# Kernel tuning notes

Hardware: AMD Instinct MI355X
Metric: run time of the kernel (lower is better)

## Reference

```python
import jax, jax.numpy as jnp
import numpy as np

# --- static config (matches init_kwargs / input_specs) ---
N_GRAPHS = 32
NODES = 1000          # num_nodes per graph
N = N_GRAPHS * NODES  # 32000 total nodes
F_IN = 128            # num_features
E_DIM = 16            # edge_attr_dim
H, C = 4, 16          # heads, GAT_dim
HC = H * C            # 64
E = 512000            # edges (before self-loops)
PROJ = 8              # proj_nodes
OUT = 256             # output_dim
NEG_SLOPE = 0.2       # PyG GATConv default


def setup_inputs() -> dict:
    key = jax.random.key(0)
    ks = jax.random.split(key, 20)
    s = 0.1
    return {
        "x": jax.random.normal(ks[0], (N, F_IN), jnp.float32),
        "edge_attr": jax.random.normal(ks[1], (E, E_DIM), jnp.float32),
        # layer 0 (input_conv): F_IN -> H*C
        "W0":   jax.random.normal(ks[2], (F_IN, HC), jnp.float32) * s,
        "a_s0": jax.random.normal(ks[3], (H, C), jnp.float32) * s,
        "a_d0": jax.random.normal(ks[4], (H, C), jnp.float32) * s,
        "W_e0": jax.random.normal(ks[5], (E_DIM, HC), jnp.float32) * s,
        "a_e0": jax.random.normal(ks[6], (H, C), jnp.float32) * s,
        "b0":   jnp.zeros((HC,), jnp.float32),
        # layers 1..2 stacked: HC -> H*C
        "Wg":   jax.random.normal(ks[7], (2, HC, HC), jnp.float32) * s,
        "a_sg": jax.random.normal(ks[8], (2, H, C), jnp.float32) * s,
        "a_dg": jax.random.normal(ks[9], (2, H, C), jnp.float32) * s,
        "W_eg": jax.random.normal(ks[10], (2, E_DIM, HC), jnp.float32) * s,
        "a_eg": jax.random.normal(ks[11], (2, H, C), jnp.float32) * s,
        "bg":   jnp.zeros((2, HC), jnp.float32),
        # node_proj: HC -> PROJ ; fc_out: NODES*PROJ -> OUT
        "Wp": jax.random.normal(ks[12], (HC, PROJ), jnp.float32) * s,
        "bp": jnp.zeros((PROJ,), jnp.float32),
        "Wo": jax.random.normal(ks[13], (NODES * PROJ, OUT), jnp.float32) * (s / 4),
        "bo": jnp.zeros((OUT,), jnp.float32),
        "edge_index": jax.random.randint(ks[14], (2, E), 0, N, jnp.int32),
        "batch": jnp.repeat(jnp.arange(N_GRAPHS, dtype=jnp.int32), NODES),
    }


def _gat_layer(x, src, dst, eattr, W, a_s, a_d, W_e, a_e, b):
    """PyG GATConv (concat=True, shared src/dst lin, edge_dim) forward."""
    xl = (x @ W).reshape(N, H, C)                       # [N,H,C]
    al_s = jnp.sum(xl * a_s, axis=-1)                   # [N,H]
    al_d = jnp.sum(xl * a_d, axis=-1)                   # [N,H]
    el = (eattr @ W_e).reshape(-1, H, C)                # [Ef,H,C]
    al_e = jnp.sum(el * a_e, axis=-1)                   # [Ef,H]
    logits = jax.nn.leaky_relu(al_s[src] + al_d[dst] + al_e, NEG_SLOPE)
    # segment softmax over destination nodes (every node has a self-loop)
    mx = jax.ops.segment_max(logits, dst, num_segments=N)
    p = jnp.exp(logits - mx[dst])
    denom = jax.ops.segment_sum(p, dst, num_segments=N)
    alpha = p / denom[dst]                               # [Ef,H]
    out = jax.ops.segment_sum(xl[src] * alpha[..., None], dst, num_segments=N)
    return out.reshape(N, HC) + b


def reference(x, edge_attr, W0, a_s0, a_d0, W_e0, a_e0, b0,
              Wg, a_sg, a_dg, W_eg, a_eg, bg,
              Wp, bp, Wo, bo, edge_index, batch):
    src, dst = edge_index[0], edge_index[1]
    # PyG add_self_loops with fill_value='mean': per-dst mean of incoming edge_attr
    deg = jax.ops.segment_sum(jnp.ones((E,), edge_attr.dtype), dst, num_segments=N)
    loop_attr = jax.ops.segment_sum(edge_attr, dst, num_segments=N) / jnp.maximum(deg, 1.0)[:, None]
    loops = jnp.arange(N, dtype=src.dtype)
    src_f = jnp.concatenate([src, loops])
    dst_f = jnp.concatenate([dst, loops])
    ea_f = jnp.concatenate([edge_attr, loop_attr], axis=0)   # [E+N, E_DIM]

    h = jax.nn.relu(_gat_layer(x, src_f, dst_f, ea_f, W0, a_s0, a_d0, W_e0, a_e0, b0))
    for i in range(2):
        h = jax.nn.relu(_gat_layer(h, src_f, dst_f, ea_f,
                                   Wg[i], a_sg[i], a_dg[i], W_eg[i], a_eg[i], bg[i]))
    h = jax.nn.relu(h @ Wp + bp)                             # [N, PROJ]
    B = batch.shape[0] // NODES                              # static batch count
    h = h.reshape(B, NODES * PROJ)
    return h @ Wo + bo                                       # [B, OUT]
```

## Files before the change

### kernel.cpp

```cpp
#include <hip/hip_runtime.h>
#include <hip/hip_bf16.h>
#include <hip/hip_fp16.h>

#define N_NODES 32000
#define FIN     128
#define E_EDGES 512000
#define EF_EDGES 544000
#define HC      64
#define NGRAPH  32
#define PROJ    8
#define OUT_DIM 256

static __device__ inline unsigned short f2bf(float f) {
  unsigned int x = __float_as_uint(f);
  unsigned int r = (x + 0x7fffu + ((x >> 16) & 1u)) >> 16;
  return (unsigned short)r;
}
static __device__ inline float bf2f(unsigned short u) {
  return __uint_as_float((unsigned int)u << 16);
}
static __device__ inline unsigned short f2h(float f) {
  return __half_as_ushort(__float2half(f));
}
static __device__ inline float h2f(unsigned short u) {
  return __half2float(__ushort_as_half(u));
}

__global__ __launch_bounds__(256) void zero_kernel(int* __restrict__ deg) {
  deg[blockIdx.x * 256 + threadIdx.x] = 0;
}

__global__ __launch_bounds__(256) void deg_kernel(const int* __restrict__ ei,
                                                  int* __restrict__ deg) {
  int e = blockIdx.x * 256 + threadIdx.x;
  atomicAdd(&deg[ei[E_EDGES + e]], 1);
}

__global__ __launch_bounds__(256) void scan1_kernel(const int* __restrict__ deg,
                                                    int* __restrict__ offs,
                                                    int* __restrict__ bsum) {
  int idx = blockIdx.x * 256 + threadIdx.x;
  int lane = threadIdx.x & 63;
  int w = threadIdx.x >> 6;
  int v = deg[idx] + 1;
  int s = v;
#pragma unroll
  for (int off = 1; off < 64; off <<= 1) {
    int t = __shfl_up(s, off);
    if (lane >= off) s += t;
  }
  __shared__ int wsum[4];
  if (lane == 63) wsum[w] = s;
  __syncthreads();
  int add = 0;
#pragma unroll
  for (int i = 0; i < 4; ++i) add += (i < w) ? wsum[i] : 0;
  int incl = s + add;
  offs[idx] = incl - v;
  if (threadIdx.x == 255) bsum[blockIdx.x] = incl;
}

__global__ __launch_bounds__(256) void scan3_kernel(const int* __restrict__ bsum,
                                                    int* __restrict__ offs,
                                                    int* __restrict__ nxt) {
  __shared__ int wsum[4];
  int tid = threadIdx.x, bid = blockIdx.x;
  int lane = tid & 63, w = tid >> 6;
  int v = (tid < bid) ? bsum[tid] : 0;
#pragma unroll
  for (int off = 1; off < 64; off <<= 1) v += __shfl_xor(v, off);
  if (lane == 0) wsum[w] = v;
  __syncthreads();
  int boff = wsum[0] + wsum[1] + wsum[2] + wsum[3];
  int idx = bid * 256 + tid;
  int o = offs[idx] + boff;
  offs[idx] = o;
  nxt[idx] = o;
  if (bid == 0 && tid == 0) offs[N_NODES] = EF_EDGES;
}

__global__ __launch_bounds__(256) void fill_kernel(const int* __restrict__ ei,
                                                   int* __restrict__ nxt,
                                                   int* __restrict__ csr_src,
                                                   int* __restrict__ csr_eid) {
  int e = blockIdx.x * 256 + threadIdx.x;
  int s, d;
  if (e < E_EDGES) { s = ei[e]; d = ei[E_EDGES + e]; }
  else             { s = e - E_EDGES; d = s; }
  int pos = atomicAdd(&nxt[d], 1);
  csr_src[pos] = s;
  csr_eid[pos] = e;
}

__device__ __forceinline__ void compute_Me(float (*sMe)[16][4],
                                           const float* __restrict__ W_e0,
                                           const float* __restrict__ a_e0,
                                           const float* __restrict__ W_eg,
                                           const float* __restrict__ a_eg) {
  int tid = threadIdx.x;
  if (tid < 192) {
    int l = tid >> 6, r6 = tid & 63, d = r6 >> 2, h = r6 & 3;
    const float* We = (l == 0) ? W_e0 : W_eg + (size_t)(l - 1) * 16 * HC;
    const float* ae = (l == 0) ? a_e0 : a_eg + (size_t)(l - 1) * 64;
    float s = 0.f;
#pragma unroll
    for (int c = 0; c < 16; ++c) s += We[d * HC + h * 16 + c] * ae[h * 16 + c];
    sMe[l][d][h] = s;
  }
  __syncthreads();
}

__global__ __launch_bounds__(256) void edge_kernel(const float* __restrict__ edge_attr,
                                                   const float* __restrict__ W_e0,
                                                   const float* __restrict__ a_e0,
                                                   const float* __restrict__ W_eg,
                                                   const float* __restrict__ a_eg,
                                                   const int* __restrict__ offs,
                                                   const int* __restrict__ csr_eid,
                                                   unsigned short* __restrict__ lgE) {
  __shared__ float sMe[3][16][4];
  __shared__ float sMean[4][16];
  compute_Me(sMe, W_e0, a_e0, W_eg, a_eg);
  int b = blockIdx.x;
  int tid = threadIdx.x;
  if (b < 8000) {
    int lane = tid & 63, wv = tid >> 6;
    int n = b * 4 + wv;
    int k = lane & 15, g = lane >> 4;
    int beg = offs[n], end = offs[n + 1];
    float s = 0.f;
    int posl = -1;
    for (int i = beg + g; i < end; i += 4) {
      int e = csr_eid[i];
      if (e < E_EDGES) s += edge_attr[(size_t)e * 16 + k];
      else posl = i;
    }
    s += __shfl_xor(s, 16);
    s += __shfl_xor(s, 32);
    posl = max(posl, __shfl_xor(posl, 16));
    posl = max(posl, __shfl_xor(posl, 32));
    int degv = end - beg - 1;
    float mean = s / fmaxf((float)degv, 1.f);
    if (g == 0) sMean[wv][k] = mean;
    if (lane < 3) {
      int l = lane;
      float r0 = 0.f, r1 = 0.f, r2 = 0.f, r3 = 0.f;
#pragma unroll
      for (int d = 0; d < 16; ++d) {
        float a = sMean[wv][d];
        r0 = fmaf(a, sMe[l][d][0], r0);
        r1 = fmaf(a, sMe[l][d][1], r1);
        r2 = fmaf(a, sMe[l][d][2], r2);
        r3 = fmaf(a, sMe[l][d][3], r3);
      }
      unsigned long long u =
          (unsigned long long)f2h(r0) |
          ((unsigned long long)f2h(r1) << 16) |
          ((unsigned long long)f2h(r2) << 32) |
          ((unsigned long long)f2h(r3) << 48);
      *(unsigned long long*)&lgE[((size_t)l * EF_EDGES + posl) * 4] = u;
    }
  } else {
    int pos = (b - 8000) * 256 + tid;
    int e = csr_eid[pos];
    if (e < E_EDGES) {
      float av[16];
      *(float4*)&av[0]  = *(const float4*)&edge_attr[(size_t)e * 16 + 0];
      *(float4*)&av[4]  = *(const float4*)&edge_attr[(size_t)e * 16 + 4];
      *(float4*)&av[8]  = *(const float4*)&edge_attr[(size_t)e * 16 + 8];
      *(float4*)&av[12] = *(const float4*)&edge_attr[(size_t)e * 16 + 12];
#pragma unroll
      for (int l = 0; l < 3; ++l) {
        float r0 = 0.f, r1 = 0.f, r2 = 0.f, r3 = 0.f;
#pragma unroll
        for (int d = 0; d < 16; ++d) {
          float a = av[d];
          r0 = fmaf(a, sMe[l][d][0], r0);
          r1 = fmaf(a, sMe[l][d][1], r1);
          r2 = fmaf(a, sMe[l][d][2], r2);
          r3 = fmaf(a, sMe[l][d][3], r3);
        }
        unsigned long long u =
            (unsigned long long)f2h(r0) |
            ((unsigned long long)f2h(r1) << 16) |
            ((unsigned long long)f2h(r2) << 32) |
            ((unsigned long long)f2h(r3) << 48);
        __builtin_nontemporal_store(
            u, (unsigned long long*)&lgE[((size_t)l * EF_EDGES + pos) * 4]);
      }
    }
  }
}

template <int K>
__global__ __launch_bounds__(256) void transform_kernel(const float* __restrict__ A,
                                                        const float* __restrict__ W,
                                                        const float* __restrict__ a_s,
                                                        const float* __restrict__ a_d,
                                                        unsigned short* __restrict__ xlb,
                                                        float* __restrict__ al_s,
                                                        float* __restrict__ al_d) {
  __shared__ float sW[64][64];
  __shared__ float sA[64][65];
  int tid = threadIdx.x;
  int row0 = blockIdx.x * 64;
  int tx = tid & 15, ty = tid >> 4;
  int c0 = tx * 4, r0 = ty * 4;
  float acc[4][4] = {};
  for (int kc = 0; kc < K; kc += 64) {
    for (int i = tid; i < 1024; i += 256) {
      int kk = i >> 4, c4 = (i & 15) * 4;
      *(float4*)&sW[kk][c4] = *(const float4*)&W[(size_t)(kc + kk) * HC + c4];
    }
    for (int i = tid; i < 1024; i += 256) {
      int r = i >> 4, k4 = (i & 15) * 4;
      float4 v = *(const float4*)&A[(size_t)(row0 + r) * K + kc + k4];
      sA[r][k4 + 0] = v.x; sA[r][k4 + 1] = v.y;
      sA[r][k4 + 2] = v.z; sA[r][k4 + 3] = v.w;
    }
    __syncthreads();
#pragma unroll 8
    for (int kk = 0; kk < 64; ++kk) {
      float4 w = *(float4*)&sW[kk][c0];
      float a0 = sA[r0 + 0][kk];
      float a1 = sA[r0 + 1][kk];
      float a2 = sA[r0 + 2][kk];
      float a3 = sA[r0 + 3][kk];
      acc[0][0] = fmaf(a0, w.x, acc[0][0]); acc[0][1] = fmaf(a0, w.y, acc[0][1]);
      acc[0][2] = fmaf(a0, w.z, acc[0][2]); acc[0][3] = fmaf(a0, w.w, acc[0][3]);
      acc[1][0] = fmaf(a1, w.x, acc[1][0]); acc[1][1] = fmaf(a1, w.y, acc[1][1]);
      acc[1][2] = fmaf(a1, w.z, acc[1][2]); acc[1][3] = fmaf(a1, w.w, acc[1][3]);
      acc[2][0] = fmaf(a2, w.x, acc[2][0]); acc[2][1] = fmaf(a2, w.y, acc[2][1]);
      acc[2][2] = fmaf(a2, w.z, acc[2][2]); acc[2][3] = fmaf(a2, w.w, acc[2][3]);
      acc[3][0] = fmaf(a3, w.x, acc[3][0]); acc[3][1] = fmaf(a3, w.y, acc[3][1]);
      acc[3][2] = fmaf(a3, w.z, acc[3][2]); acc[3][3] = fmaf(a3, w.w, acc[3][3]);
    }
    __syncthreads();
  }
  float asv[4], adv[4];
#pragma unroll
  for (int j = 0; j < 4; ++j) { asv[j] = a_s[c0 + j]; adv[j] = a_d[c0 + j]; }
  int hd = tx >> 2;
#pragma unroll
  for (int i = 0; i < 4; ++i) {
    int r = row0 + r0 + i;
    ushort4 u = make_ushort4(f2bf(acc[i][0]), f2bf(acc[i][1]),
                             f2bf(acc[i][2]), f2bf(acc[i][3]));
    *(ushort4*)&xlb[(size_t)r * HC + c0] = u;
    float ps = acc[i][0] * asv[0] + acc[i][1] * asv[1] + acc[i][2] * asv[2] + acc[i][3] * asv[3];
    float pd = acc[i][0] * adv[0] + acc[i][1] * adv[1] + acc[i][2] * adv[2] + acc[i][3] * adv[3];
    ps += __shfl_xor(ps, 1); ps += __shfl_xor(ps, 2);
    pd += __shfl_xor(pd, 1); pd += __shfl_xor(pd, 2);
    if ((tx & 3) == 0) {
      al_s[(size_t)r * 4 + hd] = ps;
      al_d[(size_t)r * 4 + hd] = pd;
    }
  }
}

template <int FUSE_PROJ>
__global__ __launch_bounds__(256) void gather_kernel(const int* __restrict__ offs,
                                                     const int* __restrict__ csr_src,
                                                     const unsigned short* __restrict__ lg,
                                                     const unsigned short* __restrict__ xlb,
                                                     const float* __restrict__ al_s,
                                                     const float* __restrict__ al_d,
                                                     const float* __restrict__ bias,
                                                     const float* __restrict__ Wp,
                                                     const float* __restrict__ bp,
                                                     float* __restrict__ outp) {
  int tid = threadIdx.x;
  int lane = tid & 63;
  int n = blockIdx.x * 4 + (tid >> 6);
  int u = lane & 31;
  int hf = lane >> 5;
  int c0 = u * 2;
  int hd = u >> 3;
  int beg = offs[n], end = offs[n + 1];
  float ald = al_d[(size_t)n * 4 + hd];
  float m = -1e30f, denom = 0.f, a0 = 0.f, a1 = 0.f;
  int ib = beg;
  for (; ib + 8 <= end; ib += 8) {
    int j0 = ib + hf, j1 = j0 + 2, j2 = j0 + 4, j3 = j0 + 6;
    int s0 = csr_src[j0];
    int s1 = csr_src[j1];
    int s2 = csr_src[j2];
    int s3 = csr_src[j3];
    unsigned short g0 = lg[(size_t)j0 * 4 + hd];
    unsigned short g1 = lg[(size_t)j1 * 4 + hd];
    unsigned short g2 = lg[(size_t)j2 * 4 + hd];
    unsigned short g3 = lg[(size_t)j3 * 4 + hd];
    unsigned int x0 = *(const unsigned int*)&xlb[(size_t)s0 * HC + c0];
    unsigned int x1 = *(const unsigned int*)&xlb[(size_t)s1 * HC + c0];
    unsigned int x2 = *(const unsigned int*)&xlb[(size_t)s2 * HC + c0];
    unsigned int x3 = *(const unsigned int*)&xlb[(size_t)s3 * HC + c0];
    float l0 = h2f(g0) + al_s[(size_t)s0 * 4 + hd] + ald;
    float l1 = h2f(g1) + al_s[(size_t)s1 * 4 + hd] + ald;
    float l2 = h2f(g2) + al_s[(size_t)s2 * 4 + hd] + ald;
    float l3 = h2f(g3) + al_s[(size_t)s3 * 4 + hd] + ald;
    l0 = (l0 > 0.f) ? l0 : 0.2f * l0;
    l1 = (l1 > 0.f) ? l1 : 0.2f * l1;
    l2 = (l2 > 0.f) ? l2 : 0.2f * l2;
    l3 = (l3 > 0.f) ? l3 : 0.2f * l3;
    float mx = fmaxf(fmaxf(fmaxf(l0, l1), fmaxf(l2, l3)), m);
    float sc = __expf(m - mx);
    float p0 = __expf(l0 - mx);
    float p1 = __expf(l1 - mx);
    float p2 = __expf(l2 - mx);
    float p3 = __expf(l3 - mx);
    denom = denom * sc + ((p0 + p1) + (p2 + p3));
    a0 = a0 * sc + p0 * bf2f((unsigned short)(x0 & 0xffff))
                 + p1 * bf2f((unsigned short)(x1 & 0xffff))
                 + p2 * bf2f((unsigned short)(x2 & 0xffff))
                 + p3 * bf2f((unsigned short)(x3 & 0xffff));
    a1 = a1 * sc + p0 * bf2f((unsigned short)(x0 >> 16))
                 + p1 * bf2f((unsigned short)(x1 >> 16))
                 + p2 * bf2f((unsigned short)(x2 >> 16))
                 + p3 * bf2f((unsigned short)(x3 >> 16));
    m = mx;
  }
  for (int j = ib + hf; j < end; j += 2) {
    int s = csr_src[j];
    unsigned short g = lg[(size_t)j * 4 + hd];
    unsigned int xx = *(const unsigned int*)&xlb[(size_t)s * HC + c0];
    float l = h2f(g) + al_s[(size_t)s * 4 + hd] + ald;
    l = (l > 0.f) ? l : 0.2f * l;
    float mx = fmaxf(m, l);
    float sc = __expf(m - mx);
    float pp = __expf(l - mx);
    denom = denom * sc + pp;
    a0 = a0 * sc + pp * bf2f((unsigned short)(xx & 0xffff));
    a1 = a1 * sc + pp * bf2f((unsigned short)(xx >> 16));
    m = mx;
  }
  float m2 = __shfl_xor(m, 32);
  float d2 = __shfl_xor(denom, 32);
  float b0 = __shfl_xor(a0, 32);
  float b1 = __shfl_xor(a1, 32);
  float mm = fmaxf(m, m2);
  float sA = __expf(m - mm), sB = __expf(m2 - mm);
  denom = denom * sA + d2 * sB;
  a0 = a0 * sA + b0 * sB;
  a1 = a1 * sA + b1 * sB;
  float hv0 = fmaxf(a0 / denom + bias[c0], 0.f);
  float hv1 = fmaxf(a1 / denom + bias[c0 + 1], 0.f);
  if constexpr (!FUSE_PROJ) {
    if (hf == 0) {
      float2 o; o.x = hv0; o.y = hv1;
      *(float2*)&outp[(size_t)n * HC + c0] = o;
    }
  } else {
    float pj[8];
#pragma unroll
    for (int j = 0; j < 8; ++j)
      pj[j] = (hf == 0) ? hv0 * Wp[c0 * PROJ + j] + hv1 * Wp[(c0 + 1) * PROJ + j] : 0.f;
#pragma unroll
    for (int off = 1; off < 64; off <<= 1) {
#pragma unroll
      for (int j = 0; j < 8; ++j) pj[j] += __shfl_xor(pj[j], off);
    }
    if (lane < 8) {
      float v = pj[0];
      v = (lane == 1) ? pj[1] : v;
      v = (lane == 2) ? pj[2] : v;
      v = (lane == 3) ? pj[3] : v;
      v = (lane == 4) ? pj[4] : v;
      v = (lane == 5) ? pj[5] : v;
      v = (lane == 6) ? pj[6] : v;
      v = (lane == 7) ? pj[7] : v;
      outp[(size_t)n * PROJ + lane] = fmaxf(v + bp[lane], 0.f);
    }
  }
}

__global__ __launch_bounds__(256) void fc1_kernel(const float* __restrict__ p,
                                                  const float* __restrict__ Wo,
                                                  float* __restrict__ part) {
  __shared__ float sp[NGRAPH][250];
  int kc = blockIdx.x;
  int ct = blockIdx.y;
  int tid = threadIdx.x;
  for (int i = tid; i < NGRAPH * 250; i += 256) {
    int g = i / 250, kk = i % 250;
    sp[g][kk] = p[(size_t)g * 8000 + kc * 250 + kk];
  }
  __syncthreads();
  int c = ct * 64 + (tid & 63);
  int kg = tid >> 6;
  float acc[NGRAPH] = {};
  for (int kk = kg; kk < 250; kk += 4) {
    float w = __builtin_nontemporal_load(&Wo[(size_t)(kc * 250 + kk) * OUT_DIM + c]);
#pragma unroll
    for (int g = 0; g < NGRAPH; ++g) acc[g] = fmaf(sp[g][kk], w, acc[g]);
  }
  int ch = kc * 4 + kg;
#pragma unroll
  for (int g = 0; g < NGRAPH; ++g)
    part[((size_t)ch * NGRAPH + g) * OUT_DIM + c] = acc[g];
}

__global__ __launch_bounds__(256) void fc2_kernel(const float* __restrict__ part,
                                                  const float* __restrict__ bo,
                                                  float* __restrict__ out) {
  int i = blockIdx.x * 256 + threadIdx.x;
  int g = i >> 8, c = i & 255;
  float s = bo[c];
  for (int ch = 0; ch < 128; ++ch) s += part[((size_t)ch * NGRAPH + g) * OUT_DIM + c];
  out[i] = s;
}

extern "C" void kernel_launch(void* const* d_in, const int* in_sizes, int n_in,
                              void* d_out, int out_size, void* d_ws, size_t ws_size,
                              hipStream_t stream) {
  const float* x         = (const float*)d_in[0];
  const float* edge_attr = (const float*)d_in[1];
  const float* W0        = (const float*)d_in[2];
  const float* a_s0      = (const float*)d_in[3];
  const float* a_d0      = (const float*)d_in[4];
  const float* W_e0      = (const float*)d_in[5];
  const float* a_e0      = (const float*)d_in[6];
  const float* b0        = (const float*)d_in[7];
  const float* Wg        = (const float*)d_in[8];
  const float* a_sg      = (const float*)d_in[9];
  const float* a_dg      = (const float*)d_in[10];
  const float* W_eg      = (const float*)d_in[11];
  const float* a_eg      = (const float*)d_in[12];
  const float* bg        = (const float*)d_in[13];
  const float* Wp        = (const float*)d_in[14];
  const float* bp        = (const float*)d_in[15];
  const float* Wo        = (const float*)d_in[16];
  const float* bo        = (const float*)d_in[17];
  const int*   ei        = (const int*)d_in[18];

  char* base = (char*)d_ws;
  size_t off = 0;
  auto alloc = [&](size_t bytes) -> void* {
    void* ptr = base + off;
    off = (off + bytes + 255) & ~(size_t)255;
    return ptr;
  };
  int*            deg     = (int*)alloc((size_t)N_NODES * 4);
  int*            offs    = (int*)alloc((size_t)(N_NODES + 1) * 4);
  int*            nxt     = (int*)alloc((size_t)N_NODES * 4);
  int*            bsum    = (int*)alloc(128 * 4);
  int*            csr_src = (int*)alloc((size_t)EF_EDGES * 4);
  int*            csr_eid = (int*)alloc((size_t)EF_EDGES * 4);
  unsigned short* lgE     = (unsigned short*)alloc((size_t)3 * EF_EDGES * 4 * 2);
  unsigned short* xlb     = (unsigned short*)alloc((size_t)N_NODES * HC * 2);
  float*          al_s    = (float*)alloc((size_t)N_NODES * 4 * 4);
  float*          al_d    = (float*)alloc((size_t)N_NODES * 4 * 4);
  float*          hA      = (float*)alloc((size_t)N_NODES * HC * 4);
  float*          hB      = (float*)alloc((size_t)N_NODES * HC * 4);
  float*          pbuf    = (float*)alloc((size_t)N_NODES * PROJ * 4);
  float*          part    = (float*)alloc((size_t)128 * NGRAPH * OUT_DIM * 4);

  zero_kernel<<<N_NODES / 256, 256, 0, stream>>>(deg);
  deg_kernel<<<E_EDGES / 256, 256, 0, stream>>>(ei, deg);
  scan1_kernel<<<N_NODES / 256, 256, 0, stream>>>(deg, offs, bsum);
  scan3_kernel<<<N_NODES / 256, 256, 0, stream>>>(bsum, offs, nxt);
  fill_kernel<<<EF_EDGES / 256, 256, 0, stream>>>(ei, nxt, csr_src, csr_eid);
  edge_kernel<<<8000 + 2125, 256, 0, stream>>>(edge_attr, W_e0, a_e0, W_eg, a_eg,
                                               offs, csr_eid, lgE);
  transform_kernel<FIN><<<N_NODES / 64, 256, 0, stream>>>(x, W0, a_s0, a_d0, xlb, al_s, al_d);

  gather_kernel<0><<<N_NODES / 4, 256, 0, stream>>>(offs, csr_src, lgE, xlb,
                                                    al_s, al_d, b0, Wp, bp, hA);
  transform_kernel<HC><<<N_NODES / 64, 256, 0, stream>>>(hA, Wg, a_sg, a_dg, xlb, al_s, al_d);
  gather_kernel<0><<<N_NODES / 4, 256, 0, stream>>>(offs, csr_src, lgE + (size_t)EF_EDGES * 4,
                                                    xlb, al_s, al_d, bg, Wp, bp, hB);
  transform_kernel<HC><<<N_NODES / 64, 256, 0, stream>>>(hB, Wg + HC * HC, a_sg + 64,
                                                         a_dg + 64, xlb, al_s, al_d);
  gather_kernel<1><<<N_NODES / 4, 256, 0, stream>>>(offs, csr_src, lgE + (size_t)2 * EF_EDGES * 4,
                                                    xlb, al_s, al_d, bg + 64, Wp, bp, pbuf);

  fc1_kernel<<<dim3(32, 4), 256, 0, stream>>>(pbuf, Wo, part);
  fc2_kernel<<<NGRAPH, 256, 0, stream>>>(part, bo, (float*)d_out);
}
```

Before: 274.5 us.

## Pack source attention scores into feature rows and drop online softmax max

Stores the per-head source attention logit inside each node's bf16 feature row, padded to a stride of 72, so the gather reads features and al_s from the same row instead of from two separate arrays. The softmax no longer subtracts a running maximum, which removes the rescaling exps and lets the half-wave merge become a plain sum. The edge loop is unrolled to 16 edges per iteration, with loads batched ahead of the math to raise memory-level parallelism. The risk is overflow in exp if logits grow large, since there is no max subtraction.

New measurement: 278.6 us. No clear change (+1.5%).

```diff
diff --git a/kernel.cpp b/kernel.cpp
--- a/kernel.cpp
+++ b/kernel.cpp
@@ -7,6 +7,7 @@
 #define E_EDGES 512000
 #define EF_EDGES 544000
 #define HC      64
+#define XSTR    72
 #define NGRAPH  32
 #define PROJ    8
 #define OUT_DIM 256
@@ -198,7 +199,6 @@
                                                         const float* __restrict__ a_s,
                                                         const float* __restrict__ a_d,
                                                         unsigned short* __restrict__ xlb,
-                                                        float* __restrict__ al_s,
                                                         float* __restrict__ al_d) {
   __shared__ float sW[64][64];
   __shared__ float sA[64][65];
@@ -246,13 +246,13 @@
     int r = row0 + r0 + i;
     ushort4 u = make_ushort4(f2bf(acc[i][0]), f2bf(acc[i][1]),
                              f2bf(acc[i][2]), f2bf(acc[i][3]));
-    *(ushort4*)&xlb[(size_t)r * HC + c0] = u;
+    *(ushort4*)&xlb[(size_t)r * XSTR + c0] = u;
     float ps = acc[i][0] * asv[0] + acc[i][1] * asv[1] + acc[i][2] * asv[2] + acc[i][3] * asv[3];
     float pd = acc[i][0] * adv[0] + acc[i][1] * adv[1] + acc[i][2] * adv[2] + acc[i][3] * adv[3];
     ps += __shfl_xor(ps, 1); ps += __shfl_xor(ps, 2);
     pd += __shfl_xor(pd, 1); pd += __shfl_xor(pd, 2);
     if ((tx & 3) == 0) {
-      al_s[(size_t)r * 4 + hd] = ps;
+      *(float*)&xlb[(size_t)r * XSTR + 64 + hd * 2] = ps;
       al_d[(size_t)r * 4 + hd] = pd;
     }
   }
@@ -263,7 +263,6 @@
                                                      const int* __restrict__ csr_src,
                                                      const unsigned short* __restrict__ lg,
                                                      const unsigned short* __restrict__ xlb,
-                                                     const float* __restrict__ al_s,
                                                      const float* __restrict__ al_d,
                                                      const float* __restrict__ bias,
                                                      const float* __restrict__ Wp,
@@ -278,70 +277,49 @@
   int hd = u >> 3;
   int beg = offs[n], end = offs[n + 1];
   float ald = al_d[(size_t)n * 4 + hd];
-  float m = -1e30f, denom = 0.f, a0 = 0.f, a1 = 0.f;
+  float denom = 0.f, a0 = 0.f, a1 = 0.f;
   int ib = beg;
-  for (; ib + 8 <= end; ib += 8) {
-    int j0 = ib + hf, j1 = j0 + 2, j2 = j0 + 4, j3 = j0 + 6;
-    int s0 = csr_src[j0];
-    int s1 = csr_src[j1];
-    int s2 = csr_src[j2];
-    int s3 = csr_src[j3];
-    unsigned short g0 = lg[(size_t)j0 * 4 + hd];
-    unsigned short g1 = lg[(size_t)j1 * 4 + hd];
-    unsigned short g2 = lg[(size_t)j2 * 4 + hd];
-    unsigned short g3 = lg[(size_t)j3 * 4 + hd];
-    unsigned int x0 = *(const unsigned int*)&xlb[(size_t)s0 * HC + c0];
-    unsigned int x1 = *(const unsigned int*)&xlb[(size_t)s1 * HC + c0];
-    unsigned int x2 = *(const unsigned int*)&xlb[(size_t)s2 * HC + c0];
-    unsigned int x3 = *(const unsigned int*)&xlb[(size_t)s3 * HC + c0];
-    float l0 = h2f(g0) + al_s[(size_t)s0 * 4 + hd] + ald;
-    float l1 = h2f(g1) + al_s[(size_t)s1 * 4 + hd] + ald;
-    float l2 = h2f(g2) + al_s[(size_t)s2 * 4 + hd] + ald;
-    float l3 = h2f(g3) + al_s[(size_t)s3 * 4 + hd] + ald;
-    l0 = (l0 > 0.f) ? l0 : 0.2f * l0;
-    l1 = (l1 > 0.f) ? l1 : 0.2f * l1;
-    l2 = (l2 > 0.f) ? l2 : 0.2f * l2;
-    l3 = (l3 > 0.f) ? l3 : 0.2f * l3;
-    float mx = fmaxf(fmaxf(fmaxf(l0, l1), fmaxf(l2, l3)), m);
-    float sc = __expf(m - mx);
-    float p0 = __expf(l0 - mx);
-    float p1 = __expf(l1 - mx);
-    float p2 = __expf(l2 - mx);
-    float p3 = __expf(l3 - mx);
-    denom = denom * sc + ((p0 + p1) + (p2 + p3));
-    a0 = a0 * sc + p0 * bf2f((unsigned short)(x0 & 0xffff))
-                 + p1 * bf2f((unsigned short)(x1 & 0xffff))
-                 + p2 * bf2f((unsigned short)(x2 & 0xffff))
-                 + p3 * bf2f((unsigned short)(x3 & 0xffff));
-    a1 = a1 * sc + p0 * bf2f((unsigned short)(x0 >> 16))
-                 + p1 * bf2f((unsigned short)(x1 >> 16))
-                 + p2 * bf2f((unsigned short)(x2 >> 16))
-                 + p3 * bf2f((unsigned short)(x3 >> 16));
-    m = mx;
+  for (; ib + 16 <= end; ib += 16) {
+    int sq[8]; unsigned short gq[8];
+#pragma unroll
+    for (int q = 0; q < 8; ++q) {
+      int j = ib + hf + q * 2;
+      sq[q] = csr_src[j];
+      gq[q] = lg[(size_t)j * 4 + hd];
+    }
+    unsigned int xq[8]; float alsq[8];
+#pragma unroll
+    for (int q = 0; q < 8; ++q) {
+      const unsigned short* row = &xlb[(size_t)sq[q] * XSTR];
+      xq[q] = *(const unsigned int*)&row[c0];
+      alsq[q] = *(const float*)&row[64 + hd * 2];
+    }
+#pragma unroll
+    for (int q = 0; q < 8; ++q) {
+      float l = h2f(gq[q]) + alsq[q] + ald;
+      l = (l > 0.f) ? l : 0.2f * l;
+      float p = __expf(l);
+      denom += p;
+      a0 = fmaf(p, bf2f((unsigned short)(xq[q] & 0xffff)), a0);
+      a1 = fmaf(p, bf2f((unsigned short)(xq[q] >> 16)), a1);
+    }
   }
   for (int j = ib + hf; j < end; j += 2) {
     int s = csr_src[j];
     unsigned short g = lg[(size_t)j * 4 + hd];
-    unsigned int xx = *(const unsigned int*)&xlb[(size_t)s * HC + c0];
-    float l = h2f(g) + al_s[(size_t)s * 4 + hd] + ald;
+    const unsigned short* row = &xlb[(size_t)s * XSTR];
+    unsigned int xx = *(const unsigned int*)&row[c0];
+    float als = *(const float*)&row[64 + hd * 2];
+    float l = h2f(g) + als + ald;
     l = (l > 0.f) ? l : 0.2f * l;
-    float mx = fmaxf(m, l);
-    float sc = __expf(m - mx);
-    float pp = __expf(l - mx);
-    denom = denom * sc + pp;
-    a0 = a0 * sc + pp * bf2f((unsigned short)(xx & 0xffff));
-    a1 = a1 * sc + pp * bf2f((unsigned short)(xx >> 16));
-    m = mx;
-  }
-  float m2 = __shfl_xor(m, 32);
-  float d2 = __shfl_xor(denom, 32);
-  float b0 = __shfl_xor(a0, 32);
-  float b1 = __shfl_xor(a1, 32);
-  float mm = fmaxf(m, m2);
-  float sA = __expf(m - mm), sB = __expf(m2 - mm);
-  denom = denom * sA + d2 * sB;
-  a0 = a0 * sA + b0 * sB;
-  a1 = a1 * sA + b1 * sB;
+    float p = __expf(l);
+    denom += p;
+    a0 = fmaf(p, bf2f((unsigned short)(xx & 0xffff)), a0);
+    a1 = fmaf(p, bf2f((unsigned short)(xx >> 16)), a1);
+  }
+  denom += __shfl_xor(denom, 32);
+  a0 += __shfl_xor(a0, 32);
+  a1 += __shfl_xor(a1, 32);
   float hv0 = fmaxf(a0 / denom + bias[c0], 0.f);
   float hv1 = fmaxf(a1 / denom + bias[c0 + 1], 0.f);
   if constexpr (!FUSE_PROJ) {
@@ -446,8 +424,7 @@
   int*            csr_src = (int*)alloc((size_t)EF_EDGES * 4);
   int*            csr_eid = (int*)alloc((size_t)EF_EDGES * 4);
   unsigned short* lgE     = (unsigned short*)alloc((size_t)3 * EF_EDGES * 4 * 2);
-  unsigned short* xlb     = (unsigned short*)alloc((size_t)N_NODES * HC * 2);
-  float*          al_s    = (float*)alloc((size_t)N_NODES * 4 * 4);
+  unsigned short* xlb     = (unsigned short*)alloc((size_t)N_NODES * XSTR * 2);
   float*          al_d    = (float*)alloc((size_t)N_NODES * 4 * 4);
   float*          hA      = (float*)alloc((size_t)N_NODES * HC * 4);
   float*          hB      = (float*)alloc((size_t)N_NODES * HC * 4);
@@ -461,17 +438,17 @@
   fill_kernel<<<EF_EDGES / 256, 256, 0, stream>>>(ei, nxt, csr_src, csr_eid);
   edge_kernel<<<8000 + 2125, 256, 0, stream>>>(edge_attr, W_e0, a_e0, W_eg, a_eg,
                                                offs, csr_eid, lgE);
-  transform_kernel<FIN><<<N_NODES / 64, 256, 0, stream>>>(x, W0, a_s0, a_d0, xlb, al_s, al_d);
+  transform_kernel<FIN><<<N_NODES / 64, 256, 0, stream>>>(x, W0, a_s0, a_d0, xlb, al_d);
 
   gather_kernel<0><<<N_NODES / 4, 256, 0, stream>>>(offs, csr_src, lgE, xlb,
-                                                    al_s, al_d, b0, Wp, bp, hA);
-  transform_kernel<HC><<<N_NODES / 64, 256, 0, stream>>>(hA, Wg, a_sg, a_dg, xlb, al_s, al_d);
+                                                    al_d, b0, Wp, bp, hA);
+  transform_kernel<HC><<<N_NODES / 64, 256, 0, stream>>>(hA, Wg, a_sg, a_dg, xlb, al_d);
   gather_kernel<0><<<N_NODES / 4, 256, 0, stream>>>(offs, csr_src, lgE + (size_t)EF_EDGES * 4,
-                                                    xlb, al_s, al_d, bg, Wp, bp, hB);
+                                                    xlb, al_d, bg, Wp, bp, hB);
   transform_kernel<HC><<<N_NODES / 64, 256, 0, stream>>>(hB, Wg + HC * HC, a_sg + 64,
-                                                         a_dg + 64, xlb, al_s, al_d);
+                                                         a_dg + 64, xlb, al_d);
   gather_kernel<1><<<N_NODES / 4, 256, 0, stream>>>(offs, csr_src, lgE + (size_t)2 * EF_EDGES * 4,
-                                                    xlb, al_s, al_d, bg + 64, Wp, bp, pbuf);
+                                                    xlb, al_d, bg + 64, Wp, bp, pbuf);
 
   fc1_kernel<<<dim3(32, 4), 256, 0, stream>>>(pbuf, Wo, part);
   fc2_kernel<<<NGRAPH, 256, 0, stream>>>(part, bo, (float*)d_out);
```
